# Optimization experiments

Hardware: AMD Instinct MI355X
Metric: run time of the kernel (lower is better)

Reference implementation:

```python
import jax, jax.numpy as jnp
import numpy as np

B, T, D, H = 4, 2048, 1024, 16
HD = D // H


def setup_inputs() -> dict:
    key = jax.random.key(0)
    ks = jax.random.split(key, 6)
    x = jax.random.normal(ks[0], (B, T, D), dtype=jnp.float32)
    entity_bias = jax.random.normal(ks[1], (B, T, T), dtype=jnp.float32) * 0.02
    W_qkv = jax.random.normal(ks[2], (D, 3 * D), dtype=jnp.float32) * (1.0 / np.sqrt(D))
    b_qkv = jnp.zeros((3 * D,), dtype=jnp.float32)
    W_out = jax.random.normal(ks[3], (D, D), dtype=jnp.float32) * (1.0 / np.sqrt(D))
    b_out = jnp.zeros((D,), dtype=jnp.float32)
    return {"x": x, "entity_bias": entity_bias, "W_qkv": W_qkv, "b_qkv": b_qkv,
            "W_out": W_out, "b_out": b_out}


def reference(x, entity_bias, W_qkv, b_qkv, W_out, b_out):
    b, t, d = x.shape
    hd = d // H
    scale = hd ** -0.5
    qkv = x @ W_qkv + b_qkv                      # [B,T,3D]
    q, k, v = jnp.split(qkv, 3, axis=-1)
    sh = lambda z: z.reshape(b, t, H, hd).transpose(0, 2, 1, 3)  # [B,H,T,hd]
    q, k, v = sh(q), sh(k), sh(v)
    w = jnp.einsum('bhqd,bhkd->bhqk', q, k) * scale
    w = w + entity_bias[:, None]                 # broadcast over heads
    causal = jnp.triu(jnp.ones((t, t), dtype=bool), k=1)
    w = jnp.where(causal[None, None], jnp.float32(-1e9), w)
    a = jax.nn.softmax(w, axis=-1)
    out = jnp.einsum('bhqk,bhkd->bhqd', a, v)    # [B,H,T,hd]
    out = out.transpose(0, 2, 1, 3).reshape(b, t, d)
    return out @ W_out + b_out
```

## Files before the change

### kernel.cpp

```cpp
#include <hip/hip_runtime.h>

typedef __attribute__((ext_vector_type(8))) short short8;
typedef __attribute__((ext_vector_type(4))) short short4v;
typedef __attribute__((ext_vector_type(4))) float f32x4;

#define B_  4
#define T_  2048
#define D_  1024
#define H_  16
#define HD_ 64

#define LOG2E 1.4426950408889634f
#define QSCALE 0.1803368801111243f

__device__ __forceinline__ short f2bf(float f) {
  unsigned u = __builtin_bit_cast(unsigned, f);
  u = (u + 0x7FFFu + ((u >> 16) & 1u)) >> 16;
  return (short)u;
}
__device__ __forceinline__ short f2bf_trunc(float f) {
  return (short)(__builtin_bit_cast(unsigned, f) >> 16);
}
__device__ __forceinline__ float bf2f(short s) {
  unsigned u = ((unsigned)(unsigned short)s) << 16;
  return __builtin_bit_cast(float, u);
}

__device__ __forceinline__ void g2l16(const void* g, void* l) {
  __builtin_amdgcn_global_load_lds((const __attribute__((address_space(1))) void*)g,
                                   (__attribute__((address_space(3))) void*)l, 16, 0, 0);
}

__global__ __launch_bounds__(512) void prep_kernel(const float* __restrict__ x,
                                                   short* __restrict__ xb,
                                                   const float* __restrict__ bias,
                                                   short* __restrict__ PB) {
  int bid = blockIdx.x;
  if (bid < 4096) {
    int i = (bid * 512 + threadIdx.x) * 4;
    float4 v = *(const float4*)(x + i);
    short4v o;
    o.x = f2bf(v.x); o.y = f2bf(v.y); o.z = f2bf(v.z); o.w = f2bf(v.w);
    *(short4v*)(xb + i) = o;
    return;
  }
  bid -= 4096;
  int b = bid / 136, tidx = bid % 136;
  int qt = 0, base = 0;
  while (base + qt + 1 <= tidx) { base += qt + 1; ++qt; }
  int kt = tidx - base;
  int tid = threadIdx.x;
  int w = tid >> 6, lane = tid & 63, quad = lane >> 4, l15 = lane & 15;
  short vals[32];
#pragma unroll
  for (int tj = 0; tj < 8; ++tj)
#pragma unroll
    for (int rr = 0; rr < 4; ++rr) {
      int ql = w * 16 + quad * 4 + rr;
      int kl = tj * 16 + l15;
      float v = bias[((size_t)b * T_ + qt * 128 + ql) * T_ + kt * 128 + kl] * LOG2E;
      if (kt == qt && kl > ql) v = -1.0e9f;
      vals[tj * 4 + rr] = f2bf(v);
    }
  short* dst = PB + ((size_t)bid * 512 + tid) * 32;
#pragma unroll
  for (int j = 0; j < 4; ++j) *(short8*)(dst + j * 8) = *(const short8*)(vals + j * 8);
}

__device__ __forceinline__ void tcast_body(const float* __restrict__ src,
                                           short* __restrict__ dst, int R, int C,
                                           int cb, int rb, float tile[32][33]) {
  int tr = threadIdx.x >> 5, tc = threadIdx.x & 31;
#pragma unroll
  for (int p = 0; p < 4; ++p) {
    int r = p * 8 + tr;
    tile[r][tc] = src[(size_t)(rb * 32 + r) * C + cb * 32 + tc];
  }
  __syncthreads();
#pragma unroll
  for (int p = 0; p < 4; ++p) {
    int r = p * 8 + tr;
    dst[(size_t)(cb * 32 + r) * R + rb * 32 + tc] = f2bf(tile[tc][r]);
  }
}

__global__ __launch_bounds__(256) void tcast2_kernel(const float* __restrict__ Wqkv,
                                                     const float* __restrict__ Wout,
                                                     short* __restrict__ Wqt,
                                                     short* __restrict__ Wot) {
  __shared__ float tile[32][33];
  int cb = blockIdx.x, rb = blockIdx.y;
  if (cb < 96) tcast_body(Wqkv, Wqt, 1024, 3072, cb, rb, tile);
  else         tcast_body(Wout, Wot, 1024, 1024, cb - 96, rb, tile);
}

__device__ __forceinline__ void gemm_stage(const short* __restrict__ A,
                                           const short* __restrict__ Bt, int K, int mb, int nb,
                                           int kk, short* As, short* Bs, int wave, int lane) {
#pragma unroll
  for (int i = 0; i < 2; ++i) {
    int sbase = i * 256 + wave * 64;
    int s = sbase + lane;
    int r = s >> 2;
    int cg = (s & 3) ^ ((s >> 3) & 3);
    g2l16(A + (size_t)(mb * 128 + r) * K + kk * 32 + cg * 8, As + sbase * 8);
    g2l16(Bt + (size_t)(nb * 128 + r) * K + kk * 32 + cg * 8, Bs + sbase * 8);
  }
}

__device__ __forceinline__ void gemm_compute(const short* As, const short* Bs, f32x4 acc[4][4],
                                             int quad, int l15, int wr, int wc) {
  short8 af[4], bq[4];
  int sw = quad ^ ((l15 >> 1) & 3);
#pragma unroll
  for (int t = 0; t < 4; ++t) {
    af[t] = *(const short8*)(As + ((wr * 64 + t * 16 + l15) * 4 + sw) * 8);
    bq[t] = *(const short8*)(Bs + ((wc * 64 + t * 16 + l15) * 4 + sw) * 8);
  }
#pragma unroll
  for (int i = 0; i < 4; ++i)
#pragma unroll
    for (int j = 0; j < 4; ++j)
      acc[i][j] = __builtin_amdgcn_mfma_f32_16x16x32_bf16(af[i], bq[j], acc[i][j], 0, 0, 0);
}

__device__ __forceinline__ void gemm_core(const short* __restrict__ A, const short* __restrict__ Bt,
                                          int K, int mb, int nb, short* As, short* Bs,
                                          f32x4 acc[4][4]) {
  const int tid = threadIdx.x;
  const int wave = tid >> 6, lane = tid & 63;
  const int quad = lane >> 4, l15 = lane & 15;
  const int wr = wave >> 1, wc = wave & 1;
  f32x4 zero = {0.f, 0.f, 0.f, 0.f};
#pragma unroll
  for (int i = 0; i < 4; ++i)
#pragma unroll
    for (int j = 0; j < 4; ++j) acc[i][j] = zero;

  const int nK = K >> 5;
  gemm_stage(A, Bt, K, mb, nb, 0, As, Bs, wave, lane);
  __syncthreads();
  for (int kk = 0; kk < nK - 1; ++kk) {
    int cur = kk & 1;
    gemm_stage(A, Bt, K, mb, nb, kk + 1, As + (cur ^ 1) * 4096, Bs + (cur ^ 1) * 4096, wave, lane);
    gemm_compute(As + cur * 4096, Bs + cur * 4096, acc, quad, l15, wr, wc);
    __syncthreads();
  }
  gemm_compute(As + ((nK - 1) & 1) * 4096, Bs + ((nK - 1) & 1) * 4096, acc, quad, l15, wr, wc);
}

__global__ __launch_bounds__(256, 4) void gemm_qkv_kernel(
    const short* __restrict__ xb, const short* __restrict__ Wqt, const float* __restrict__ bqkv,
    short* __restrict__ Qb, short* __restrict__ Kb, short* __restrict__ Vt) {
  __shared__ alignas(16) short As[2 * 4096];
  __shared__ alignas(16) short Bs[2 * 4096];
  f32x4 acc[4][4];
  int nb = blockIdx.x, mb = blockIdx.y;
  gemm_core(xb, Wqt, D_, mb, nb, As, Bs, acc);

  const int tid = threadIdx.x, wave = tid >> 6, lane = tid & 63;
  const int quad = lane >> 4, l15 = lane & 15;
  const int wr = wave >> 1, wc = wave & 1;
  int part = nb >> 3;
  int h = ((nb & 7) << 1) + wc;
  if (part == 2) {
#pragma unroll
    for (int j = 0; j < 4; ++j) {
      int n = nb * 128 + wc * 64 + j * 16 + l15;
      int hd = j * 16 + l15;
      float bv = bqkv[n];
#pragma unroll
      for (int i = 0; i < 4; ++i) {
        int m0 = mb * 128 + wr * 64 + i * 16 + quad * 4;
        int b = m0 >> 11, t0 = m0 & 2047;
        short4v pv;
#pragma unroll
        for (int rr = 0; rr < 4; ++rr) pv[rr] = f2bf(acc[i][j][rr] + bv);
        *(short4v*)(Vt + ((size_t)((b * H_ + h) * HD_ + hd)) * T_ + t0) = pv;
      }
    }
  } else {
    short* dst = (part == 0) ? Qb : Kb;
    float sc = (part == 0) ? QSCALE : 1.0f;
#pragma unroll
    for (int j = 0; j < 4; ++j) {
      int n = nb * 128 + wc * 64 + j * 16 + l15;
      int hd = j * 16 + l15;
      float bv = bqkv[n];
#pragma unroll
      for (int i = 0; i < 4; ++i) {
        int mrow = mb * 128 + wr * 64 + i * 16 + quad * 4;
#pragma unroll
        for (int rr = 0; rr < 4; ++rr) {
          int m = mrow + rr;
          int b = m >> 11, t = m & 2047;
          dst[((size_t)((b * H_ + h) * T_ + t)) * HD_ + hd] = f2bf((acc[i][j][rr] + bv) * sc);
        }
      }
    }
  }
}

__global__ __launch_bounds__(256, 4) void gemm_out_kernel(
    const short* __restrict__ Ob, const short* __restrict__ Wot,
    const float* __restrict__ bout, float* __restrict__ out) {
  __shared__ alignas(16) short As[2 * 4096];
  __shared__ alignas(16) short Bs[2 * 4096];
  f32x4 acc[4][4];
  int nb = blockIdx.x, mb = blockIdx.y;
  gemm_core(Ob, Wot, D_, mb, nb, As, Bs, acc);

  const int tid = threadIdx.x, wave = tid >> 6, lane = tid & 63;
  const int quad = lane >> 4, l15 = lane & 15;
  const int wr = wave >> 1, wc = wave & 1;
#pragma unroll
  for (int j = 0; j < 4; ++j) {
    int n = nb * 128 + wc * 64 + j * 16 + l15;
    float bv = bout[n];
#pragma unroll
    for (int i = 0; i < 4; ++i) {
      int mrow = mb * 128 + wr * 64 + i * 16 + quad * 4;
#pragma unroll
      for (int rr = 0; rr < 4; ++rr) {
        out[(size_t)(mrow + rr) * D_ + n] = acc[i][j][rr] + bv;
      }
    }
  }
}

__global__ __launch_bounds__(512, 2) void attn_kernel(
    const short* __restrict__ Qb, const short* __restrict__ Kb, const short* __restrict__ Vt,
    const short* __restrict__ PB, short* __restrict__ Ob) {
  __shared__ alignas(16) short Ks[2][8192];
  __shared__ alignas(16) short Vs[2][8192];
  __shared__ alignas(16) short Ps[8][512];

  const int tid = threadIdx.x, wave = tid >> 6, lane = tid & 63;
  const int quad = lane >> 4, l15 = lane & 15;
  const int bh = blockIdx.x;
  const int pair = blockIdx.y;
  const int qa = pair, qb = 15 - pair;
  const int b = bh >> 4, h = bh & 15;

  short8 aqA[2], aqB[2];
#pragma unroll
  for (int i = 0; i < 2; ++i) {
    int sbase = i * 512 + wave * 64;
    int s = sbase + lane;
    int r = s >> 3;
    int cg = (s & 7) ^ (r & 7);
    g2l16(Qb + ((size_t)bh * T_ + qa * 128 + r) * HD_ + cg * 8, &Ks[0][0] + sbase * 8);
    g2l16(Qb + ((size_t)bh * T_ + qb * 128 + r) * HD_ + cg * 8, &Vs[0][0] + sbase * 8);
  }
  __syncthreads();
  {
    int qrow = wave * 16 + l15;
#pragma unroll
    for (int c2 = 0; c2 < 2; ++c2) {
      int ch = (c2 * 4 + quad) ^ (l15 & 7);
      aqA[c2] = *(const short8*)(&Ks[0][0] + (qrow * 8 + ch) * 8);
      aqB[c2] = *(const short8*)(&Vs[0][0] + (qrow * 8 + ch) * 8);
    }
  }
  __syncthreads();

  f32x4 zero = {0.f, 0.f, 0.f, 0.f};
  f32x4 oA[4], oB[4];
  float liA[4], liB[4];
#pragma unroll
  for (int hj = 0; hj < 4; ++hj) { oA[hj] = zero; oB[hj] = zero; }
#pragma unroll
  for (int rr = 0; rr < 4; ++rr) { liA[rr] = 0.f; liB[rr] = 0.f; }

  const short* pbA = PB + ((size_t)(b * 136 + ((qa * (qa + 1)) >> 1)) * 512 + tid) * 32;
  const short* pbB = PB + ((size_t)(b * 136 + ((qb * (qb + 1)) >> 1)) * 512 + tid) * 32;
  short* pw = &Ps[wave][0];

  auto stage_kv = [&](int kt, int bufc) {
#pragma unroll
    for (int i = 0; i < 2; ++i) {
      int sbase = i * 512 + wave * 64;
      int s = sbase + lane;
      int rk = s >> 3, ck = (s & 7) ^ ((s >> 3) & 7);
      g2l16(Kb + ((size_t)bh * T_ + kt * 128 + rk) * HD_ + ck * 8, &Ks[bufc][0] + sbase * 8);
      int rv = s >> 4, cv = (s & 15) ^ ((s >> 4) & 7);
      g2l16(Vt + ((size_t)bh * HD_ + rv) * T_ + kt * 128 + cv * 8, &Vs[bufc][0] + sbase * 8);
    }
  };

  auto attn_step = [&](int kt, int bufc) {
    const short* Ksc = &Ks[bufc][0];
    const short* Vsc = &Vs[bufc][0];
    const int ks0 = quad ^ (l15 & 7), ks1 = ks0 ^ 4;
    const int vsw = l15 & 7;
#pragma unroll
    for (int tile = 0; tile < 2; ++tile) {
      if (tile == 1 && kt > qa) break;
      const short* pp = (tile == 0 ? pbB : pbA) + (size_t)kt * (512 * 32);
      const short8* aq = (tile == 0) ? aqB : aqA;
      f32x4* o = (tile == 0) ? oB : oA;
      float* li = (tile == 0) ? liB : liA;

#pragma unroll 1
      for (int half = 0; half < 2; ++half) {
        f32x4 sc[4];
#pragma unroll
        for (int j4 = 0; j4 < 2; ++j4) {
          short8 pb = *(const short8*)(pp + (half * 2 + j4) * 8);
#pragma unroll
          for (int tp = 0; tp < 2; ++tp)
#pragma unroll
            for (int rr = 0; rr < 4; ++rr) sc[j4 * 2 + tp][rr] = bf2f(pb[tp * 4 + rr]);
        }
#pragma unroll
        for (int tj = 0; tj < 4; ++tj) {
          int key = (half * 4 + tj) * 16 + l15;
          short8 bk0 = *(const short8*)(Ksc + (key * 8 + ks0) * 8);
          short8 bk1 = *(const short8*)(Ksc + (key * 8 + ks1) * 8);
          sc[tj] = __builtin_amdgcn_mfma_f32_16x16x32_bf16(aq[0], bk0, sc[tj], 0, 0, 0);
          sc[tj] = __builtin_amdgcn_mfma_f32_16x16x32_bf16(aq[1], bk1, sc[tj], 0, 0, 0);
        }

#pragma unroll
        for (int tj = 0; tj < 4; ++tj)
#pragma unroll
          for (int rr = 0; rr < 4; ++rr) {
            float p = __builtin_amdgcn_exp2f(sc[tj][rr]);
            sc[tj][rr] = p;
            li[rr] += p;
          }

#pragma unroll
        for (int kc = 0; kc < 2; ++kc) {
          int kcc = half * 2 + kc;
#pragma unroll
          for (int tp = 0; tp < 2; ++tp) {
            int tj = kc * 2 + tp;
            int klc = tp * 16 + l15;
            int hi = (klc >> 3) * 16;
#pragma unroll
            for (int rr = 0; rr < 4; ++rr) {
              pw[(hi + quad * 4 + rr) * 8 + (klc & 7)] = f2bf_trunc(sc[tj][rr]);
            }
          }
          short8 ap = *(const short8*)(pw + (quad * 16 + l15) * 8);
#pragma unroll
          for (int hj = 0; hj < 4; ++hj) {
            int hd = hj * 16 + l15;
            int tc = (kcc * 4 + quad) ^ vsw;
            short8 bv = *(const short8*)(Vsc + (hd * 16 + tc) * 8);
            o[hj] = __builtin_amdgcn_mfma_f32_16x16x32_bf16(ap, bv, o[hj], 0, 0, 0);
          }
        }
      }
    }
  };

  stage_kv(0, 0);
  __syncthreads();
  for (int kt = 0; kt < qb; ++kt) {
    int cur = kt & 1;
    stage_kv(kt + 1, cur ^ 1);
    attn_step(kt, cur);
    __syncthreads();
  }
  attn_step(qb, qb & 1);

#pragma unroll
  for (int d = 1; d < 16; d <<= 1)
#pragma unroll
    for (int rr = 0; rr < 4; ++rr) {
      liA[rr] += __shfl_xor(liA[rr], d, 64);
      liB[rr] += __shfl_xor(liB[rr], d, 64);
    }

#pragma unroll
  for (int hj = 0; hj < 4; ++hj)
#pragma unroll
    for (int rr = 0; rr < 4; ++rr) {
      int qrow = wave * 16 + quad * 4 + rr;
      int dcol = h * 64 + hj * 16 + l15;
      Ob[((size_t)b * T_ + qa * 128 + qrow) * D_ + dcol] = f2bf(oA[hj][rr] / liA[rr]);
      Ob[((size_t)b * T_ + qb * 128 + qrow) * D_ + dcol] = f2bf(oB[hj][rr] / liB[rr]);
    }
}

extern "C" void kernel_launch(void* const* d_in, const int* in_sizes, int n_in,
                              void* d_out, int out_size, void* d_ws, size_t ws_size,
                              hipStream_t stream) {
  const float* x    = (const float*)d_in[0];
  const float* bias = (const float*)d_in[1];
  const float* Wqkv = (const float*)d_in[2];
  const float* bqkv = (const float*)d_in[3];
  const float* Wout = (const float*)d_in[4];
  const float* bout = (const float*)d_in[5];
  float* out = (float*)d_out;
  char* ws = (char*)d_ws;

  short* xb   = (short*)(ws + 0);
  short* Ob   = (short*)(ws + 0);
  short* Wqt  = (short*)(ws + 16777216);
  short* Wot  = (short*)(ws + 23068672);
  short* Qb   = (short*)(ws + 25165824);
  short* Kb   = (short*)(ws + 41943040);
  short* Vt   = (short*)(ws + 58720256);
  short* PB   = (short*)(ws + 75497472);

  prep_kernel<<<4640, 512, 0, stream>>>(x, xb, bias, PB);
  tcast2_kernel<<<dim3(128, 32), 256, 0, stream>>>(Wqkv, Wout, Wqt, Wot);
  gemm_qkv_kernel<<<dim3(24, 64), 256, 0, stream>>>(xb, Wqt, bqkv, Qb, Kb, Vt);
  attn_kernel<<<dim3(64, 8), 512, 0, stream>>>(Qb, Kb, Vt, PB, Ob);
  gemm_out_kernel<<<dim3(8, 64), 256, 0, stream>>>(Ob, Wot, bout, out);
}
```

Measured before the change: 329.0 us.

## Stage QKV GEMM epilogue through LDS for coalesced 16-byte stores and remap block order

The QKV projection epilogue now writes bf16 results into a padded shared-memory tile, then each thread stores contiguous 128-byte rows to Q, K and transposed V using 16-byte vector writes. This replaces scattered 2-byte global stores. The block index is also remapped so that consecutive blocks are spread across M tiles, which changes L2 reuse and the grouping across XCDs. It costs an extra LDS round trip and two more barriers per block.

Result: slower. 336.3 us (+2.2%).

```diff
diff --git a/kernel.cpp b/kernel.cpp
--- a/kernel.cpp
+++ b/kernel.cpp
@@ -152,51 +152,73 @@
 __global__ __launch_bounds__(256, 4) void gemm_qkv_kernel(
     const short* __restrict__ xb, const short* __restrict__ Wqt, const float* __restrict__ bqkv,
     short* __restrict__ Qb, short* __restrict__ Kb, short* __restrict__ Vt) {
-  __shared__ alignas(16) short As[2 * 4096];
-  __shared__ alignas(16) short Bs[2 * 4096];
+  __shared__ alignas(16) short S[17408];
   f32x4 acc[4][4];
-  int nb = blockIdx.x, mb = blockIdx.y;
-  gemm_core(xb, Wqt, D_, mb, nb, As, Bs, acc);
+  int lid = blockIdx.y * 24 + blockIdx.x;
+  int nlid = (lid & 7) * 192 + (lid >> 3);
+  int nb = nlid % 24, mb = nlid / 24;
+  gemm_core(xb, Wqt, D_, mb, nb, S, S + 8192, acc);
 
   const int tid = threadIdx.x, wave = tid >> 6, lane = tid & 63;
   const int quad = lane >> 4, l15 = lane & 15;
   const int wr = wave >> 1, wc = wave & 1;
   int part = nb >> 3;
-  int h = ((nb & 7) << 1) + wc;
+
+  __syncthreads();
+
   if (part == 2) {
 #pragma unroll
     for (int j = 0; j < 4; ++j) {
-      int n = nb * 128 + wc * 64 + j * 16 + l15;
-      int hd = j * 16 + l15;
-      float bv = bqkv[n];
+      int n = wc * 64 + j * 16 + l15;
+      float bv = bqkv[nb * 128 + n];
 #pragma unroll
       for (int i = 0; i < 4; ++i) {
-        int m0 = mb * 128 + wr * 64 + i * 16 + quad * 4;
-        int b = m0 >> 11, t0 = m0 & 2047;
+        int m0 = wr * 64 + i * 16 + quad * 4;
         short4v pv;
 #pragma unroll
         for (int rr = 0; rr < 4; ++rr) pv[rr] = f2bf(acc[i][j][rr] + bv);
-        *(short4v*)(Vt + ((size_t)((b * H_ + h) * HD_ + hd)) * T_ + t0) = pv;
+        *(short4v*)(S + n * 136 + m0) = pv;
       }
     }
+    __syncthreads();
+    {
+      int n = tid >> 1, hm = tid & 1;
+      int hd = n & 63, h = ((nb & 7) << 1) + (n >> 6);
+      int mg = mb * 128;
+      int b = mg >> 11;
+      int t0 = (mg & 2047) + hm * 64;
+      short* dst = Vt + ((size_t)((b * H_ + h) * HD_ + hd)) * T_ + t0;
+      const short* src = S + n * 136 + hm * 64;
+#pragma unroll
+      for (int k = 0; k < 8; ++k)
+        *(short8*)(dst + k * 8) = *(const short8*)(src + k * 8);
+    }
   } else {
-    short* dst = (part == 0) ? Qb : Kb;
+    short* qk = (part == 0) ? Qb : Kb;
     float sc = (part == 0) ? QSCALE : 1.0f;
 #pragma unroll
     for (int j = 0; j < 4; ++j) {
-      int n = nb * 128 + wc * 64 + j * 16 + l15;
-      int hd = j * 16 + l15;
-      float bv = bqkv[n];
+      int n = wc * 64 + j * 16 + l15;
+      float bv = bqkv[nb * 128 + n];
 #pragma unroll
       for (int i = 0; i < 4; ++i) {
-        int mrow = mb * 128 + wr * 64 + i * 16 + quad * 4;
-#pragma unroll
-        for (int rr = 0; rr < 4; ++rr) {
-          int m = mrow + rr;
-          int b = m >> 11, t = m & 2047;
-          dst[((size_t)((b * H_ + h) * T_ + t)) * HD_ + hd] = f2bf((acc[i][j][rr] + bv) * sc);
-        }
+        int m0 = wr * 64 + i * 16 + quad * 4;
+#pragma unroll
+        for (int rr = 0; rr < 4; ++rr)
+          S[(m0 + rr) * 136 + n] = f2bf((acc[i][j][rr] + bv) * sc);
       }
+    }
+    __syncthreads();
+    {
+      int m = tid >> 1, half = tid & 1;
+      int mg = mb * 128 + m;
+      int b = mg >> 11, t = mg & 2047;
+      int h = ((nb & 7) << 1) + half;
+      short* dst = qk + ((size_t)((b * H_ + h) * T_ + t)) * HD_;
+      const short* src = S + m * 136 + half * 64;
+#pragma unroll
+      for (int k = 0; k < 8; ++k)
+        *(short8*)(dst + k * 8) = *(const short8*)(src + k * 8);
     }
   }
 }
```
